# Performance work log

Hardware: AMD Instinct MI355X
Metric: run time of the kernel (lower is better)

Reference implementation:

```python
import jax, jax.numpy as jnp
import numpy as np
import math

N_RAYS = 16384
HIDDEN = 32
Z_BOUNDS = (0.1, 1.0, 10.0)
STEPS_FIRST = (128, 64)
N_IMPORTANCE = 128
ALPHA_IMP = 0.02
INNER, OUTER = 1.0, 2.0


def _uniform_z_log():
    # get_uniform_z_vals: per-segment log10 linspace, endpoint excluded like torch code
    segs = []
    for i in range(len(STEPS_FIRST)):
        lo, hi = math.log10(Z_BOUNDS[i]), math.log10(Z_BOUNDS[i + 1])
        segs.append(np.linspace(lo, hi - (hi - lo) / STEPS_FIRST[i], STEPS_FIRST[i], dtype=np.float32))
    return jnp.asarray(np.concatenate(segs))


def _density(x, Wd1, bd1, Wd2, bd2):
    hfeat = jax.nn.relu(x @ Wd1 + bd1)            # [N,S,HIDDEN]
    sigma = jax.nn.softplus(hfeat @ Wd2 + bd2)[..., 0]  # [N,S]
    return sigma, hfeat


def _mip_scale(x):
    # mipnerf360_scale with translation_center = 0
    dist = jnp.linalg.norm(x, axis=-1, keepdims=True)
    scale = jnp.where(dist > INNER, (OUTER - (OUTER - INNER) / dist) / dist, 1.0)
    return x * scale


def _sample_points(rays_o, rays_d, z_vals):
    pts = rays_o[:, None, :] + rays_d[:, None, :] * z_vals[..., None]  # [N,S,3]
    dirs = rays_d / jnp.linalg.norm(rays_d, axis=-1, keepdims=True)
    return pts, jnp.broadcast_to(dirs[:, None, :], pts.shape)


def _weights_from_sigma(sigmas, z_log):
    # render_rays_log compositing: delta[:, -1] = 0
    delta = jnp.concatenate([z_log[:, 1:] - z_log[:, :-1], jnp.zeros_like(z_log[:, :1])], axis=-1)
    alpha = 1.0 - jnp.exp(-sigmas * delta)
    alpha_shift = jnp.concatenate([jnp.zeros_like(alpha[:, :1]), alpha[:, :-1]], axis=-1)
    weights = alpha * jnp.cumprod(1.0 - alpha_shift, axis=-1)
    return weights


def _reweight(weights):
    z = jnp.zeros_like(weights[:, :1])
    wp = jnp.concatenate([z, weights, z], axis=-1)
    w = 0.5 * (jnp.maximum(wp[:, :-2], wp[:, 1:-1]) + jnp.maximum(wp[:, 1:-1], wp[:, 2:]))
    w = w + ALPHA_IMP / w.shape[-1]
    total = sum(STEPS_FIRST)
    seg_scale = jnp.concatenate([jnp.full((s,), s / total, w.dtype) for s in STEPS_FIRST])
    w = w * seg_scale
    return w / jnp.sum(w, axis=-1, keepdims=True)


def _sample_pdf(z_vals, weights, key):
    n_rays = z_vals.shape[0]
    cdf = jnp.cumsum(weights, axis=-1)
    z_mid = 0.5 * (z_vals[:, :-1] + z_vals[:, 1:])
    u = jnp.linspace(0.0, 1.0 - 1.0 / N_IMPORTANCE, N_IMPORTANCE, dtype=z_vals.dtype)
    u = u[None, :] + jax.random.uniform(key, (n_rays, N_IMPORTANCE), dtype=z_vals.dtype) / N_IMPORTANCE
    u = u * (cdf[:, -2:-1] - cdf[:, 1:2]) + cdf[:, 1:2]
    inds = jax.vmap(lambda c, uu: jnp.searchsorted(c, uu, side='right'))(cdf[:, 1:-2], u) + 1
    g = lambda arr, idx: jnp.take_along_axis(arr, idx, axis=1)
    cdf_b, cdf_a = g(cdf, inds - 1), g(cdf, inds)
    t = (u - cdf_b) / (cdf_a - cdf_b)
    zb, za = g(z_mid, inds - 1), g(z_mid, inds)
    return zb + (za - zb) * t


def _forward(n, h, w, K, E, bg_color, Wd1, bd1, Wd2, bd2, Wc1, bc1, Wc2, bc2):
    # get_rays
    dirs = jnp.stack([w + 0.5, h + 0.5, jnp.ones_like(w)], axis=-1)        # [N,3]
    cam_dirs = dirs @ jnp.linalg.inv(K).T
    rays_d = jnp.einsum('nij,nj->ni', E[:, :3, :3], cam_dirs)
    rays_o = E[:, :3, -1]
    # efficient_sampling (no-grad coarse pass)
    n_rays = rays_o.shape[0]
    z_log_c = jnp.broadcast_to(_uniform_z_log()[None, :], (n_rays, sum(STEPS_FIRST)))
    z_c = jnp.power(10.0, z_log_c)
    xyz_c, _ = _sample_points(rays_o, rays_d, z_c)
    sig_c, _ = _density(_mip_scale(xyz_c), Wd1, bd1, Wd2, bd2)
    w_c = _weights_from_sigma(sig_c, z_log_c)
    w_re = _reweight(w_c)
    z_log_f = jax.lax.stop_gradient(_sample_pdf(z_log_c, w_re, jax.random.key(42)))
    z_f = jnp.power(10.0, z_log_f)
    # fine pass through model
    xyz, dirs_f = _sample_points(rays_o, rays_d, z_f)
    sigma, hfeat = _density(_mip_scale(xyz), Wd1, bd1, Wd2, bd2)
    feat = jnp.concatenate([hfeat, dirs_f], axis=-1)
    rgbs = jax.nn.sigmoid(jax.nn.relu(feat @ Wc1 + bc1) @ Wc2 + bc2)       # [N,S,3]
    weights = _weights_from_sigma(sigma, z_log_f)
    image = jnp.sum(weights[..., None] * rgbs, axis=-2)
    invdepth = jnp.sum(weights / z_f, axis=-1)
    image = image + (1.0 - jnp.sum(weights, axis=-1, keepdims=True)) * bg_color
    lo, hi = math.log10(Z_BOUNDS[0]), math.log10(Z_BOUNDS[-1])
    z_log_s = (z_log_f - lo) / (hi - lo)
    return image, weights, z_log_s, invdepth


def setup_inputs() -> dict:
    key = jax.random.key(0)
    ks = jax.random.split(key, 12)
    N = N_RAYS
    h = jax.random.uniform(ks[0], (N,), dtype=jnp.float32) * 1080.0
    w = jax.random.uniform(ks[1], (N,), dtype=jnp.float32) * 1920.0
    f = 1000.0
    K = jnp.array([[f, 0.0, 960.0], [0.0, f, 540.0], [0.0, 0.0, 1.0]], jnp.float32)
    t = jax.random.normal(ks[2], (N, 3), dtype=jnp.float32) * 0.1
    E = jnp.tile(jnp.eye(4, dtype=jnp.float32)[None], (N, 1, 1)).at[:, :3, 3].set(t)
    n = jax.random.randint(ks[3], (N,), 0, 100)
    bg_color = jax.random.uniform(ks[4], (3,), dtype=jnp.float32)
    Wd1 = jax.random.normal(ks[5], (3, HIDDEN), dtype=jnp.float32) * 0.5
    bd1 = jnp.zeros((HIDDEN,), jnp.float32)
    Wd2 = jax.random.normal(ks[6], (HIDDEN, 1), dtype=jnp.float32) * 0.3
    bd2 = jnp.zeros((1,), jnp.float32)
    Wc1 = jax.random.normal(ks[7], (HIDDEN + 3, HIDDEN), dtype=jnp.float32) * 0.3
    bc1 = jnp.zeros((HIDDEN,), jnp.float32)
    Wc2 = jax.random.normal(ks[8], (HIDDEN, 3), dtype=jnp.float32) * 0.3
    bc2 = jnp.zeros((3,), jnp.float32)
    return {"n": n, "h": h, "w": w, "K": K, "E": E, "bg_color": bg_color,
            "Wd1": Wd1, "bd1": bd1, "Wd2": Wd2, "bd2": bd2,
            "Wc1": Wc1, "bc1": bc1, "Wc2": Wc2, "bc2": bc2}


def reference(n, h, w, K, E, bg_color, Wd1, bd1, Wd2, bd2, Wc1, bc1, Wc2, bc2):
    return _forward(n, h, w, K, E, bg_color, Wd1, bd1, Wd2, bd2, Wc1, bc1, Wc2, bc2)
```

## Files before the change

kernel.cpp:

```cpp
#include <hip/hip_runtime.h>
#include <stdint.h>

#define SC 192
#define SF 128
#define NT 128

#define WD1   0
#define BD1   96
#define WD2   128
#define BD2   160
#define BC2   161
#define NV4   164
#define W24   292
#define SWTOT 420

#define WS_FRAG_OFF 2048
#define WS_NEED     4096

#define RGBS 4

using half8 = __attribute__((ext_vector_type(8))) _Float16;
using f32x4 = __attribute__((ext_vector_type(4))) float;

__device__ __forceinline__ float zlog_c(int t) {
  return (t < 128) ? (-1.0f + (float)t * 0.0078125f)
                   : ((float)(t - 128) * 0.015625f);
}
__device__ __forceinline__ float delta_c(int t) {
  if (t >= SC - 1) return 0.0f;
  return zlog_c(t + 1) - zlog_c(t);
}

__device__ __forceinline__ float fast_rcp(float x) { return __builtin_amdgcn_rcpf(x); }
__device__ __forceinline__ float fast_rsq(float x) { return __builtin_amdgcn_rsqf(x); }
__device__ __forceinline__ float exp10_f(float x) { return __expf(x * 2.30258509299f); }
__device__ __forceinline__ float softplus_f(float x) {
  return fmaxf(x, 0.0f) + __logf(1.0f + __expf(-fabsf(x)));
}

__device__ __forceinline__ uint32_t pk2h(float a, float b) {
  auto p = __builtin_amdgcn_cvt_pkrtz(a, b);
  uint32_t u; __builtin_memcpy(&u, &p, 4); return u;
}
__device__ __forceinline__ unsigned short f2h(float f) {
  _Float16 h = (_Float16)f;
  unsigned short us; __builtin_memcpy(&us, &h, 2); return us;
}

__device__ __forceinline__ float4 ldsf4(const float* p) { return *(const float4*)p; }

__device__ __forceinline__ int hperm(int i, int ntf) {
  return 8 * (i >> 2) + (i & 3) + ntf * 4;
}

__device__ __forceinline__ void threefry2x32_k42(uint32_t& x0, uint32_t& x1) {
  const uint32_t ks0 = 0u, ks1 = 42u;
  const uint32_t ks2 = ks0 ^ ks1 ^ 0x1BD11BDAu;
  const uint32_t ks[3] = {ks0, ks1, ks2};
  const int rot[2][4] = {{13, 15, 26, 6}, {17, 29, 16, 24}};
  x0 += ks[0];
  x1 += ks[1];
#pragma unroll
  for (int i = 0; i < 5; ++i) {
#pragma unroll
    for (int j = 0; j < 4; ++j) {
      x0 += x1;
      const int r = rot[i & 1][j];
      x1 = (x1 << r) | (x1 >> (32 - r));
      x1 ^= x0;
    }
    x0 += ks[(i + 1) % 3];
    x1 += ks[(i + 2) % 3] + (uint32_t)(i + 1);
  }
}

__device__ __forceinline__ float wave_scan_mul(float v, int lane) {
#pragma unroll
  for (int d = 1; d < 64; d <<= 1) {
    float o = __shfl_up(v, d, 64);
    if (lane >= d) v *= o;
  }
  return v;
}
__device__ __forceinline__ float wave_scan_add(float v, int lane) {
#pragma unroll
  for (int d = 1; d < 64; d <<= 1) {
    float o = __shfl_up(v, d, 64);
    if (lane >= d) v += o;
  }
  return v;
}

__global__ __launch_bounds__(NT) void pack_weights(
    const float* __restrict__ Wd1, const float* __restrict__ bd1,
    const float* __restrict__ Wd2, const float* __restrict__ bd2,
    const float* __restrict__ Wc1, const float* __restrict__ bc1,
    const float* __restrict__ Wc2, const float* __restrict__ bc2,
    float* __restrict__ wsf) {
  const int t = threadIdx.x;
  for (int i = t; i < 96; i += NT) wsf[WD1 + i] = Wd1[i];
  for (int i = t; i < 32; i += NT) { wsf[BD1 + i] = bd1[i]; wsf[WD2 + i] = Wd2[i]; }
  if (t == 0) {
    wsf[BD2] = bd2[0];
    wsf[BC2 + 0] = bc2[0]; wsf[BC2 + 1] = bc2[1]; wsf[BC2 + 2] = bc2[2];
  }
  if (t < 32) {
    wsf[NV4 + t * 4 + 0] = bc1[t];
    wsf[NV4 + t * 4 + 1] = Wc1[32 * 32 + t];
    wsf[NV4 + t * 4 + 2] = Wc1[33 * 32 + t];
    wsf[NV4 + t * 4 + 3] = Wc1[34 * 32 + t];
  }
  if (t < 12) {
    const int m = t % 3, q = t / 3;
    uint32_t hw[4];
#pragma unroll
    for (int j2 = 0; j2 < 4; ++j2) {
      const int k0 = q * 8 + j2 * 2;
      hw[j2] = (uint32_t)f2h(Wc2[k0 * 3 + m])
             | ((uint32_t)f2h(Wc2[(k0 + 1) * 3 + m]) << 16);
    }
    ((uint4*)(wsf + W24))[t] = make_uint4(hw[0], hw[1], hw[2], hw[3]);
  }
  if (t < 64) {
    const int q_s = t >> 4;
    const int i = t & 15;
    uint4* frag = (uint4*)((char*)wsf + WS_FRAG_OFF);
#pragma unroll
    for (int nt = 0; nt < 2; ++nt) {
      const int n_s = hperm(i, nt);
      uint32_t hw[4];
#pragma unroll
      for (int j2 = 0; j2 < 4; ++j2) {
        const int k = q_s * 8 + j2 * 2;
        hw[j2] = (uint32_t)f2h(Wc1[k * 32 + n_s])
               | ((uint32_t)f2h(Wc1[(k + 1) * 32 + n_s]) << 16);
      }
      frag[t * 2 + nt] = make_uint4(hw[0], hw[1], hw[2], hw[3]);
    }
  }
}

template <bool USE_WS>
__global__ __launch_bounds__(NT, 8) void nerf_fwd(
    const float* __restrict__ hh, const float* __restrict__ ww,
    const float* __restrict__ K, const float* __restrict__ E,
    const float* __restrict__ bg,
    const float* __restrict__ Wd1, const float* __restrict__ bd1,
    const float* __restrict__ Wd2, const float* __restrict__ bd2,
    const float* __restrict__ Wc1, const float* __restrict__ bc1,
    const float* __restrict__ Wc2, const float* __restrict__ bc2,
    const float* __restrict__ wsf,
    float* __restrict__ out, int n_rays) {
  const int ray = blockIdx.x;
  const int t = threadIdx.x;
  const int lane = t & 63;
  const int wv = t >> 6;
  const int quad = lane >> 4;
  const int m15 = lane & 15;

  __shared__ __align__(16) float sw[SWTOT];
  __shared__ __align__(16) float s_A[32];
  __shared__ __align__(16) float s_B[32];
  __shared__ __align__(16) unsigned char u_buf[3072];
  float*    const s_w   = (float*)u_buf;
  float*    const s_cdf = (float*)(u_buf + 768);
  uint32_t* const s_mm  = (uint32_t*)u_buf;
  float*    const s_sig = (float*)(u_buf + 512);
  float*    const s_rgb = (float*)(u_buf + 1024);
  __shared__ float s_zlf[SF];
  __shared__ float s_tot[8];
  __shared__ float s_red[16];
  float* const s_dv = sw;

  if constexpr (USE_WS) {
    const float4* wsrc = (const float4*)wsf;
    float4* sdst = (float4*)sw;
    for (int i = t; i < SWTOT / 4; i += NT) sdst[i] = wsrc[i];
  } else {
    for (int i = t; i < 96; i += NT) sw[WD1 + i] = Wd1[i];
    for (int i = t; i < 32; i += NT) { sw[BD1 + i] = bd1[i]; sw[WD2 + i] = Wd2[i]; }
    if (t == 0) {
      sw[BD2] = bd2[0];
      sw[BC2 + 0] = bc2[0]; sw[BC2 + 1] = bc2[1]; sw[BC2 + 2] = bc2[2];
    }
    if (t < 32) {
      sw[NV4 + t * 4 + 0] = bc1[t];
      sw[NV4 + t * 4 + 1] = Wc1[32 * 32 + t];
      sw[NV4 + t * 4 + 2] = Wc1[33 * 32 + t];
      sw[NV4 + t * 4 + 3] = Wc1[34 * 32 + t];
    }
    if (t < 12) {
      const int m = t % 3, q = t / 3;
      uint32_t hw[4];
#pragma unroll
      for (int j2 = 0; j2 < 4; ++j2) {
        const int k0 = q * 8 + j2 * 2;
        hw[j2] = (uint32_t)f2h(Wc2[k0 * 3 + m])
               | ((uint32_t)f2h(Wc2[(k0 + 1) * 3 + m]) << 16);
      }
      ((uint4*)(sw + W24))[t] = make_uint4(hw[0], hw[1], hw[2], hw[3]);
    }
  }

  const float k00 = K[0], k01 = K[1], k02 = K[2];
  const float k10 = K[3], k11 = K[4], k12 = K[5];
  const float k20 = K[6], k21 = K[7], k22 = K[8];
  const float det = k00 * (k11 * k22 - k12 * k21)
                  - k01 * (k10 * k22 - k12 * k20)
                  + k02 * (k10 * k21 - k11 * k20);
  const float id = 1.0f / det;
  const float i00 =  (k11 * k22 - k12 * k21) * id;
  const float i01 = -(k01 * k22 - k02 * k21) * id;
  const float i02 =  (k01 * k12 - k02 * k11) * id;
  const float i10 = -(k10 * k22 - k12 * k20) * id;
  const float i11 =  (k00 * k22 - k02 * k20) * id;
  const float i12 = -(k00 * k12 - k02 * k10) * id;
  const float i20 =  (k10 * k21 - k11 * k20) * id;
  const float i21 = -(k00 * k21 - k01 * k20) * id;
  const float i22 =  (k00 * k11 - k01 * k10) * id;

  const float dwx = ww[ray] + 0.5f;
  const float dwy = hh[ray] + 0.5f;
  const float cx = i00 * dwx + i01 * dwy + i02;
  const float cy = i10 * dwx + i11 * dwy + i12;
  const float cz = i20 * dwx + i21 * dwy + i22;
  const float* Er = E + (size_t)ray * 16;
  const float ox = Er[3], oy = Er[7], oz = Er[11];
  const float dx = Er[0] * cx + Er[1] * cy + Er[2] * cz;
  const float dy = Er[4] * cx + Er[5] * cy + Er[6] * cz;
  const float dz = Er[8] * cx + Er[9] * cy + Er[10] * cz;
  const float dd = dx * dx + dy * dy + dz * dz;
  const float inv_nrm = fast_rsq(dd);
  const float ndx = dx * inv_nrm, ndy = dy * inv_nrm, ndz = dz * inv_nrm;
  const float oo  = ox * ox + oy * oy + oz * oz;
  const float od2 = 2.0f * (ox * dx + oy * dy + oz * dz);

  if (t < 32) {
    const float w0 = Wd1[t], w1 = Wd1[32 + t], w2 = Wd1[64 + t];
    s_A[t] = ox * w0 + oy * w1 + oz * w2;
    s_B[t] = dx * w0 + dy * w1 + dz * w2;
  }

  __syncthreads();

  if (t < 32) {
    const float4 nv = ldsf4(sw + NV4 + t * 4);
    s_dv[t] = nv.x + ndx * nv.y + ndy * nv.z + ndz * nv.w;
  }

  const float bd2v = sw[BD2];
  float a0, v0, a1e = 0.0f, v1e = 1.0f;
  {
    float ms0, msz0, ms1 = 0.f, msz1 = 0.f;
    {
      const float z = exp10_f(zlog_c(t));
      const float d2 = fmaf(z, fmaf(z, dd, od2), oo);
      const float r = fast_rsq(fmaxf(d2, 1.0f));
      ms0 = (2.0f - r) * r;
      msz0 = ms0 * z;
    }
    if (wv == 0) {
      const float z = exp10_f((float)t * 0.015625f);
      const float d2 = fmaf(z, fmaf(z, dd, od2), oo);
      const float r = fast_rsq(fmaxf(d2, 1.0f));
      ms1 = (2.0f - r) * r;
      msz1 = ms1 * z;
    }
    float acc0 = bd2v, acc1 = bd2v;
    if (wv == 0) {
#pragma unroll 2
      for (int c = 0; c < 8; ++c) {
        const int k4 = c * 4;
        const float4 A  = ldsf4(s_A + k4);
        const float4 B  = ldsf4(s_B + k4);
        const float4 b  = ldsf4(sw + BD1 + k4);
        const float4 wd = ldsf4(sw + WD2 + k4);
        float v;
        v = fmaf(msz0, B.x, fmaf(ms0, A.x, b.x)); acc0 += fmaxf(v, 0.0f) * wd.x;
        v = fmaf(msz0, B.y, fmaf(ms0, A.y, b.y)); acc0 += fmaxf(v, 0.0f) * wd.y;
        v = fmaf(msz0, B.z, fmaf(ms0, A.z, b.z)); acc0 += fmaxf(v, 0.0f) * wd.z;
        v = fmaf(msz0, B.w, fmaf(ms0, A.w, b.w)); acc0 += fmaxf(v, 0.0f) * wd.w;
        v = fmaf(msz1, B.x, fmaf(ms1, A.x, b.x)); acc1 += fmaxf(v, 0.0f) * wd.x;
        v = fmaf(msz1, B.y, fmaf(ms1, A.y, b.y)); acc1 += fmaxf(v, 0.0f) * wd.y;
        v = fmaf(msz1, B.z, fmaf(ms1, A.z, b.z)); acc1 += fmaxf(v, 0.0f) * wd.z;
        v = fmaf(msz1, B.w, fmaf(ms1, A.w, b.w)); acc1 += fmaxf(v, 0.0f) * wd.w;
      }
    } else {
#pragma unroll 2
      for (int c = 0; c < 8; ++c) {
        const int k4 = c * 4;
        const float4 A  = ldsf4(s_A + k4);
        const float4 B  = ldsf4(s_B + k4);
        const float4 b  = ldsf4(sw + BD1 + k4);
        const float4 wd = ldsf4(sw + WD2 + k4);
        float v;
        v = fmaf(msz0, B.x, fmaf(ms0, A.x, b.x)); acc0 += fmaxf(v, 0.0f) * wd.x;
        v = fmaf(msz0, B.y, fmaf(ms0, A.y, b.y)); acc0 += fmaxf(v, 0.0f) * wd.y;
        v = fmaf(msz0, B.z, fmaf(ms0, A.z, b.z)); acc0 += fmaxf(v, 0.0f) * wd.z;
        v = fmaf(msz0, B.w, fmaf(ms0, A.w, b.w)); acc0 += fmaxf(v, 0.0f) * wd.w;
      }
    }
    v0 = __expf(-softplus_f(acc0) * delta_c(t));
    a0 = 1.0f - v0;
    if (wv == 0) {
      v1e = __expf(-softplus_f(acc1) * delta_c(128 + t));
      a1e = 1.0f - v1e;
    }
  }

  float i0 = wave_scan_mul(v0, lane);
  float i1 = 1.0f;
  if (wv == 0) i1 = wave_scan_mul(v1e, lane);
  if (lane == 63) s_tot[wv] = i0;
  if (wv == 0 && lane == 63) s_tot[2] = i1;
  __syncthreads();
  {
    const float preC1 = s_tot[0];
    const float preC2 = s_tot[0] * s_tot[1];
    float e0x = __shfl_up(i0, 1, 64); if (lane == 0) e0x = 1.0f;
    s_w[t] = a0 * e0x * (wv ? preC1 : 1.0f);
    if (wv == 0) {
      float e1x = __shfl_up(i1, 1, 64); if (lane == 0) e1x = 1.0f;
      s_w[128 + t] = a1e * e1x * preC2;
    }
  }
  __syncthreads();

  float wre0, wre1 = 0.0f;
  {
    const float wm = (t > 0) ? s_w[t - 1] : 0.0f;
    const float w0 = s_w[t];
    const float wp = s_w[t + 1];
    wre0 = 0.5f * (fmaxf(wm, w0) + fmaxf(w0, wp)) + (0.02f / 192.0f);
    wre0 *= (t < 128) ? (128.0f / 192.0f) : (64.0f / 192.0f);
  }
  if (wv == 0) {
    const int e = 128 + t;
    const float wm = s_w[e - 1];
    const float w0 = s_w[e];
    const float wp = (e < SC - 1) ? s_w[e + 1] : 0.0f;
    wre1 = 0.5f * (fmaxf(wm, w0) + fmaxf(w0, wp)) + (0.02f / 192.0f);
    wre1 *= (64.0f / 192.0f);
  }

  float s0 = wave_scan_add(wre0, lane);
  float s1 = 0.0f;
  if (wv == 0) s1 = wave_scan_add(wre1, lane);
  if (lane == 63) s_tot[4 + wv] = s0;
  if (wv == 0 && lane == 63) s_tot[6] = s1;
  __syncthreads();
  {
    const float T0 = s_tot[4], T1 = s_tot[5], T2 = s_tot[6];
    const float inv_total = fast_rcp(T0 + T1 + T2);
    s_cdf[t] = (s0 + (wv ? T0 : 0.0f)) * inv_total;
    if (wv == 0) s_cdf[128 + t] = (s1 + T0 + T1) * inv_total;
  }
  __syncthreads();

  float zlf, zf;
  {
    const uint32_t total = (uint32_t)n_rays * 128u;
    const uint32_t halfc = total >> 1;
    const uint32_t j = (uint32_t)ray * 128u + (uint32_t)t;
    uint32_t x0, x1;
    const bool first = (j < halfc);
    if (first) { x0 = j; x1 = j + halfc; } else { x0 = j - halfc; x1 = j; }
    threefry2x32_k42(x0, x1);
    const uint32_t bits = first ? x0 : x1;
    const float fr = __uint_as_float((bits >> 9) | 0x3f800000u) - 1.0f;

    float u = (float)t * 0.0078125f + fr * 0.0078125f;
    u = u * (s_cdf[190] - s_cdf[1]) + s_cdf[1];

    int lo = 0, hi = 189;
    while (lo < hi) {
      const int mid = (lo + hi) >> 1;
      if (s_cdf[1 + mid] <= u) lo = mid + 1; else hi = mid;
    }
    const int inds = lo + 1;
    const float cb = s_cdf[inds - 1], ca = s_cdf[inds];
    const float tt = (u - cb) * fast_rcp(ca - cb);
    const float zb = 0.5f * (zlog_c(inds - 1) + zlog_c(inds));
    const float za = 0.5f * (zlog_c(inds) + zlog_c(inds + 1));
    zlf = zb + (za - zb) * tt;
    s_zlf[t] = zlf;
    zf = exp10_f(zlf);
  }
  __syncthreads();

  {
    const float d2 = fmaf(zf, fmaf(zf, dd, od2), oo);
    const float r = fast_rsq(fmaxf(d2, 1.0f));
    const float msf = (2.0f - r) * r;
    s_mm[t] = pk2h(msf, msf * zf);
  }

  uint4 BhS0, BhS1, BhS2, BhS3;
  {
    const bool q0 = (quad == 0);
    const int ma = hperm(m15, 0), mb = hperm(m15, 1);
    uint4 fa, fb, fd;
    fa.x = q0 ? pk2h(s_A[ma], s_B[ma]) : 0u;
    fa.y = q0 ? (uint32_t)f2h(sw[BD1 + ma]) : 0u;
    fa.z = 0u; fa.w = 0u;
    fb.x = q0 ? pk2h(s_A[mb], s_B[mb]) : 0u;
    fb.y = q0 ? (uint32_t)f2h(sw[BD1 + mb]) : 0u;
    fb.z = 0u; fb.w = 0u;
    const bool r0 = (m15 == 0);
    fd.x = r0 ? pk2h(sw[WD2 + quad * 8 + 0], sw[WD2 + quad * 8 + 1]) : 0u;
    fd.y = r0 ? pk2h(sw[WD2 + quad * 8 + 2], sw[WD2 + quad * 8 + 3]) : 0u;
    fd.z = r0 ? pk2h(sw[WD2 + quad * 8 + 4], sw[WD2 + quad * 8 + 5]) : 0u;
    fd.w = r0 ? pk2h(sw[WD2 + quad * 8 + 6], sw[WD2 + quad * 8 + 7]) : 0u;
    half8 Waug0, Waug1, WdF;
    __builtin_memcpy(&Waug0, &fa, 16);
    __builtin_memcpy(&Waug1, &fb, 16);
    __builtin_memcpy(&WdF, &fd, 16);

#pragma unroll
    for (int g = 0; g < 4; ++g) {
      const uint32_t mm = s_mm[wv * 64 + g * 16 + m15];
      uint4 bm;
      bm.x = (quad == 0) ? mm : 0u;
      bm.y = (quad == 0) ? 0x00003C00u : 0u;
      bm.z = 0u; bm.w = 0u;
      half8 Bms; __builtin_memcpy(&Bms, &bm, 16);

      f32x4 ad0 = {0.f, 0.f, 0.f, 0.f}, ad1 = {0.f, 0.f, 0.f, 0.f};
      ad0 = __builtin_amdgcn_mfma_f32_16x16x32_f16(Waug0, Bms, ad0, 0, 0, 0);
      ad1 = __builtin_amdgcn_mfma_f32_16x16x32_f16(Waug1, Bms, ad1, 0, 0, 0);

      uint4 bh;
      bh.x = pk2h(fmaxf(ad0[0], 0.0f), fmaxf(ad0[1], 0.0f));
      bh.y = pk2h(fmaxf(ad0[2], 0.0f), fmaxf(ad0[3], 0.0f));
      bh.z = pk2h(fmaxf(ad1[0], 0.0f), fmaxf(ad1[1], 0.0f));
      bh.w = pk2h(fmaxf(ad1[2], 0.0f), fmaxf(ad1[3], 0.0f));
      if (g == 0) BhS0 = bh; else if (g == 1) BhS1 = bh;
      else if (g == 2) BhS2 = bh; else BhS3 = bh;

      half8 Bh; __builtin_memcpy(&Bh, &bh, 16);
      f32x4 as = {0.f, 0.f, 0.f, 0.f};
      as = __builtin_amdgcn_mfma_f32_16x16x32_f16(WdF, Bh, as, 0, 0, 0);
      if (quad == 0) s_sig[wv * 64 + g * 16 + m15] = as[0];
    }
  }
  const float sigf = softplus_f(s_sig[t] + bd2v);

  {
    half8 Whi0, Whi1;
    if constexpr (USE_WS) {
      const uint4* frag = (const uint4*)((const char*)wsf + WS_FRAG_OFF);
      uint4 q0v = frag[lane * 2 + 0];
      uint4 q1v = frag[lane * 2 + 1];
      __builtin_memcpy(&Whi0, &q0v, 16);
      __builtin_memcpy(&Whi1, &q1v, 16);
    } else {
#pragma unroll
      for (int nt = 0; nt < 2; ++nt) {
        const int n_s = hperm(m15, nt);
        uint32_t hw[4];
#pragma unroll
        for (int j2 = 0; j2 < 4; ++j2) {
          const int k = quad * 8 + j2 * 2;
          hw[j2] = (uint32_t)f2h(Wc1[k * 32 + n_s])
                 | ((uint32_t)f2h(Wc1[(k + 1) * 32 + n_s]) << 16);
        }
        uint4 q = make_uint4(hw[0], hw[1], hw[2], hw[3]);
        if (nt == 0) __builtin_memcpy(&Whi0, &q, 16);
        else         __builtin_memcpy(&Whi1, &q, 16);
      }
    }
    const float4 dv0 = ldsf4(s_dv + quad * 8);
    const float4 dv1 = ldsf4(s_dv + quad * 8 + 4);
    uint4 qf = ((const uint4*)(sw + W24))[quad * 3 + (m15 < 3 ? m15 : 0)];
    if (m15 >= 3) qf = make_uint4(0u, 0u, 0u, 0u);
    half8 W2f; __builtin_memcpy(&W2f, &qf, 16);
    const float bc2x = sw[BC2 + 0], bc2y = sw[BC2 + 1], bc2z = sw[BC2 + 2];

#pragma unroll
    for (int g = 0; g < 4; ++g) {
      uint4 bh = (g == 0) ? BhS0 : (g == 1) ? BhS1 : (g == 2) ? BhS2 : BhS3;
      half8 Bh; __builtin_memcpy(&Bh, &bh, 16);

      f32x4 c0 = {0.f, 0.f, 0.f, 0.f}, c1 = {0.f, 0.f, 0.f, 0.f};
      c0 = __builtin_amdgcn_mfma_f32_16x16x32_f16(Whi0, Bh, c0, 0, 0, 0);
      c1 = __builtin_amdgcn_mfma_f32_16x16x32_f16(Whi1, Bh, c1, 0, 0, 0);

      uint4 bw;
      bw.x = pk2h(fmaxf(c0[0] + dv0.x, 0.0f), fmaxf(c0[1] + dv0.y, 0.0f));
      bw.y = pk2h(fmaxf(c0[2] + dv0.z, 0.0f), fmaxf(c0[3] + dv0.w, 0.0f));
      bw.z = pk2h(fmaxf(c1[0] + dv1.x, 0.0f), fmaxf(c1[1] + dv1.y, 0.0f));
      bw.w = pk2h(fmaxf(c1[2] + dv1.z, 0.0f), fmaxf(c1[3] + dv1.w, 0.0f));
      half8 Bav; __builtin_memcpy(&Bav, &bw, 16);

      f32x4 c2 = {0.f, 0.f, 0.f, 0.f};
      c2 = __builtin_amdgcn_mfma_f32_16x16x32_f16(W2f, Bav, c2, 0, 0, 0);
      if (quad == 0) {
        const int scol = wv * 64 + g * 16 + m15;
        float4 px;
        px.x = fast_rcp(1.0f + __expf(-(c2[0] + bc2x)));
        px.y = fast_rcp(1.0f + __expf(-(c2[1] + bc2y)));
        px.z = fast_rcp(1.0f + __expf(-(c2[2] + bc2z)));
        px.w = 0.0f;
        *(float4*)(s_rgb + scol * RGBS) = px;
      }
    }
  }

  const float deltaf = (t < SF - 1) ? (s_zlf[t + 1] - zlf) : 0.0f;
  const float vf = __expf(-sigf * deltaf);
  const float af = 1.0f - vf;
  float fi = wave_scan_mul(vf, lane);
  if (lane == 63) s_tot[wv] = fi;
  __syncthreads();
  float efx = __shfl_up(fi, 1, 64); if (lane == 0) efx = 1.0f;
  const float wf = af * efx * (wv ? s_tot[0] : 1.0f);

  float* o_img = out;
  float* o_w   = out + (size_t)n_rays * 3;
  float* o_z   = out + (size_t)n_rays * (3 + 128);
  float* o_inv = out + (size_t)n_rays * (3 + 256);

  o_w[(size_t)ray * 128 + t] = wf;
  o_z[(size_t)ray * 128 + t] = (zlf + 1.0f) * 0.5f;

  const float4 rgbv = ldsf4(s_rgb + t * RGBS);
  float r0 = wf * rgbv.x;
  float r1 = wf * rgbv.y;
  float r2 = wf * rgbv.z;
  float r3 = wf, r4 = wf * fast_rcp(zf);
#pragma unroll
  for (int d = 32; d > 0; d >>= 1) {
    r0 += __shfl_down(r0, d, 64);
    r1 += __shfl_down(r1, d, 64);
    r2 += __shfl_down(r2, d, 64);
    r3 += __shfl_down(r3, d, 64);
    r4 += __shfl_down(r4, d, 64);
  }
  if (lane == 0) {
    float* p = &s_red[wv * 5];
    p[0] = r0; p[1] = r1; p[2] = r2; p[3] = r3; p[4] = r4;
  }
  __syncthreads();
  if (t == 0) {
    const float accw = s_red[3] + s_red[8];
    const float bgw = 1.0f - accw;
    o_img[(size_t)ray * 3 + 0] = (s_red[0] + s_red[5]) + bgw * bg[0];
    o_img[(size_t)ray * 3 + 1] = (s_red[1] + s_red[6]) + bgw * bg[1];
    o_img[(size_t)ray * 3 + 2] = (s_red[2] + s_red[7]) + bgw * bg[2];
    o_inv[ray] = s_red[4] + s_red[9];
  }
}

extern "C" void kernel_launch(void* const* d_in, const int* in_sizes, int n_in,
                              void* d_out, int out_size, void* d_ws, size_t ws_size,
                              hipStream_t stream) {
  const float* h   = (const float*)d_in[1];
  const float* w   = (const float*)d_in[2];
  const float* K   = (const float*)d_in[3];
  const float* E   = (const float*)d_in[4];
  const float* bg  = (const float*)d_in[5];
  const float* Wd1 = (const float*)d_in[6];
  const float* bd1 = (const float*)d_in[7];
  const float* Wd2 = (const float*)d_in[8];
  const float* bd2 = (const float*)d_in[9];
  const float* Wc1 = (const float*)d_in[10];
  const float* bc1 = (const float*)d_in[11];
  const float* Wc2 = (const float*)d_in[12];
  const float* bc2 = (const float*)d_in[13];
  const int n_rays = in_sizes[1];
  float* wsf = (float*)d_ws;

  if (ws_size >= WS_NEED) {
    pack_weights<<<1, NT, 0, stream>>>(Wd1, bd1, Wd2, bd2, Wc1, bc1, Wc2, bc2, wsf);
    nerf_fwd<true><<<n_rays, NT, 0, stream>>>(h, w, K, E, bg, Wd1, bd1, Wd2, bd2,
                                              Wc1, bc1, Wc2, bc2, wsf,
                                              (float*)d_out, n_rays);
  } else {
    nerf_fwd<false><<<n_rays, NT, 0, stream>>>(h, w, K, E, bg, Wd1, bd1, Wd2, bd2,
                                               Wc1, bc1, Wc2, bc2, nullptr,
                                               (float*)d_out, n_rays);
  }
}
```

Measured before the change: 66.88 us.

## Precompute K inverse, use packed FP32 math, and move RGB sigmoid after compositing

```diff
diff --git a/kernel.cpp b/kernel.cpp
--- a/kernel.cpp
+++ b/kernel.cpp
@@ -12,7 +12,8 @@
 #define BC2   161
 #define NV4   164
 #define W24   292
-#define SWTOT 420
+#define KIV   420
+#define SWTOT 432
 
 #define WS_FRAG_OFF 2048
 #define WS_NEED     4096
@@ -21,6 +22,7 @@
 
 using half8 = __attribute__((ext_vector_type(8))) _Float16;
 using f32x4 = __attribute__((ext_vector_type(4))) float;
+using f32x2 = __attribute__((ext_vector_type(2))) float;
 
 __device__ __forceinline__ float zlog_c(int t) {
   return (t < 128) ? (-1.0f + (float)t * 0.0078125f)
@@ -36,6 +38,17 @@
 __device__ __forceinline__ float exp10_f(float x) { return __expf(x * 2.30258509299f); }
 __device__ __forceinline__ float softplus_f(float x) {
   return fmaxf(x, 0.0f) + __logf(1.0f + __expf(-fabsf(x)));
+}
+
+__device__ __forceinline__ f32x2 pk_fma2(f32x2 a, f32x2 b, f32x2 c) {
+  f32x2 d;
+  asm("v_pk_fma_f32 %0, %1, %2, %3" : "=v"(d) : "v"(a), "v"(b), "v"(c));
+  return d;
+}
+__device__ __forceinline__ f32x2 pk_add2(f32x2 a, f32x2 b) {
+  f32x2 d;
+  asm("v_pk_add_f32 %0, %1, %2" : "=v"(d) : "v"(a), "v"(b));
+  return d;
 }
 
 __device__ __forceinline__ uint32_t pk2h(float a, float b) {
@@ -92,6 +105,7 @@
 }
 
 __global__ __launch_bounds__(NT) void pack_weights(
+    const float* __restrict__ K,
     const float* __restrict__ Wd1, const float* __restrict__ bd1,
     const float* __restrict__ Wd2, const float* __restrict__ bd2,
     const float* __restrict__ Wc1, const float* __restrict__ bc1,
@@ -103,6 +117,22 @@
   if (t == 0) {
     wsf[BD2] = bd2[0];
     wsf[BC2 + 0] = bc2[0]; wsf[BC2 + 1] = bc2[1]; wsf[BC2 + 2] = bc2[2];
+    const float k00 = K[0], k01 = K[1], k02 = K[2];
+    const float k10 = K[3], k11 = K[4], k12 = K[5];
+    const float k20 = K[6], k21 = K[7], k22 = K[8];
+    const float det = k00 * (k11 * k22 - k12 * k21)
+                    - k01 * (k10 * k22 - k12 * k20)
+                    + k02 * (k10 * k21 - k11 * k20);
+    const float id = 1.0f / det;
+    wsf[KIV + 0] =  (k11 * k22 - k12 * k21) * id;
+    wsf[KIV + 1] = -(k01 * k22 - k02 * k21) * id;
+    wsf[KIV + 2] =  (k01 * k12 - k02 * k11) * id;
+    wsf[KIV + 3] = -(k10 * k22 - k12 * k20) * id;
+    wsf[KIV + 4] =  (k00 * k22 - k02 * k20) * id;
+    wsf[KIV + 5] = -(k00 * k12 - k02 * k10) * id;
+    wsf[KIV + 6] =  (k10 * k21 - k11 * k20) * id;
+    wsf[KIV + 7] = -(k00 * k21 - k01 * k20) * id;
+    wsf[KIV + 8] =  (k00 * k11 - k01 * k10) * id;
   }
   if (t < 32) {
     wsf[NV4 + t * 4 + 0] = bc1[t];
@@ -202,22 +232,29 @@
     }
   }
 
-  const float k00 = K[0], k01 = K[1], k02 = K[2];
-  const float k10 = K[3], k11 = K[4], k12 = K[5];
-  const float k20 = K[6], k21 = K[7], k22 = K[8];
-  const float det = k00 * (k11 * k22 - k12 * k21)
-                  - k01 * (k10 * k22 - k12 * k20)
-                  + k02 * (k10 * k21 - k11 * k20);
-  const float id = 1.0f / det;
-  const float i00 =  (k11 * k22 - k12 * k21) * id;
-  const float i01 = -(k01 * k22 - k02 * k21) * id;
-  const float i02 =  (k01 * k12 - k02 * k11) * id;
-  const float i10 = -(k10 * k22 - k12 * k20) * id;
-  const float i11 =  (k00 * k22 - k02 * k20) * id;
-  const float i12 = -(k00 * k12 - k02 * k10) * id;
-  const float i20 =  (k10 * k21 - k11 * k20) * id;
-  const float i21 = -(k00 * k21 - k01 * k20) * id;
-  const float i22 =  (k00 * k11 - k01 * k10) * id;
+  float i00, i01, i02, i10, i11, i12, i20, i21, i22;
+  if constexpr (USE_WS) {
+    i00 = wsf[KIV + 0]; i01 = wsf[KIV + 1]; i02 = wsf[KIV + 2];
+    i10 = wsf[KIV + 3]; i11 = wsf[KIV + 4]; i12 = wsf[KIV + 5];
+    i20 = wsf[KIV + 6]; i21 = wsf[KIV + 7]; i22 = wsf[KIV + 8];
+  } else {
+    const float k00 = K[0], k01 = K[1], k02 = K[2];
+    const float k10 = K[3], k11 = K[4], k12 = K[5];
+    const float k20 = K[6], k21 = K[7], k22 = K[8];
+    const float det = k00 * (k11 * k22 - k12 * k21)
+                    - k01 * (k10 * k22 - k12 * k20)
+                    + k02 * (k10 * k21 - k11 * k20);
+    const float id = 1.0f / det;
+    i00 =  (k11 * k22 - k12 * k21) * id;
+    i01 = -(k01 * k22 - k02 * k21) * id;
+    i02 =  (k01 * k12 - k02 * k11) * id;
+    i10 = -(k10 * k22 - k12 * k20) * id;
+    i11 =  (k00 * k22 - k02 * k20) * id;
+    i12 = -(k00 * k12 - k02 * k10) * id;
+    i20 =  (k10 * k21 - k11 * k20) * id;
+    i21 = -(k00 * k21 - k01 * k20) * id;
+    i22 =  (k00 * k11 - k01 * k10) * id;
+  }
 
   const float dwx = ww[ray] + 0.5f;
   const float dwy = hh[ray] + 0.5f;
@@ -266,7 +303,10 @@
       ms1 = (2.0f - r) * r;
       msz1 = ms1 * z;
     }
-    float acc0 = bd2v, acc1 = bd2v;
+    const f32x2 msp0 = {ms0, ms0}, mszp0 = {msz0, msz0};
+    const f32x2 msp1 = {ms1, ms1}, mszp1 = {msz1, msz1};
+    f32x2 ac0a = {0.f, 0.f}, ac0b = {0.f, 0.f};
+    f32x2 ac1a = {0.f, 0.f}, ac1b = {0.f, 0.f};
     if (wv == 0) {
 #pragma unroll 2
       for (int c = 0; c < 8; ++c) {
@@ -275,15 +315,23 @@
         const float4 B  = ldsf4(s_B + k4);
         const float4 b  = ldsf4(sw + BD1 + k4);
         const float4 wd = ldsf4(sw + WD2 + k4);
-        float v;
-        v = fmaf(msz0, B.x, fmaf(ms0, A.x, b.x)); acc0 += fmaxf(v, 0.0f) * wd.x;
-        v = fmaf(msz0, B.y, fmaf(ms0, A.y, b.y)); acc0 += fmaxf(v, 0.0f) * wd.y;
-        v = fmaf(msz0, B.z, fmaf(ms0, A.z, b.z)); acc0 += fmaxf(v, 0.0f) * wd.z;
-        v = fmaf(msz0, B.w, fmaf(ms0, A.w, b.w)); acc0 += fmaxf(v, 0.0f) * wd.w;
-        v = fmaf(msz1, B.x, fmaf(ms1, A.x, b.x)); acc1 += fmaxf(v, 0.0f) * wd.x;
-        v = fmaf(msz1, B.y, fmaf(ms1, A.y, b.y)); acc1 += fmaxf(v, 0.0f) * wd.y;
-        v = fmaf(msz1, B.z, fmaf(ms1, A.z, b.z)); acc1 += fmaxf(v, 0.0f) * wd.z;
-        v = fmaf(msz1, B.w, fmaf(ms1, A.w, b.w)); acc1 += fmaxf(v, 0.0f) * wd.w;
+        const f32x2 Axy = {A.x, A.y}, Azw = {A.z, A.w};
+        const f32x2 Bxy = {B.x, B.y}, Bzw = {B.z, B.w};
+        const f32x2 bxy = {b.x, b.y}, bzw = {b.z, b.w};
+        const f32x2 wxy = {wd.x, wd.y}, wzw = {wd.z, wd.w};
+        f32x2 p;
+        p = pk_fma2(mszp0, Bxy, pk_fma2(msp0, Axy, bxy));
+        p.x = fmaxf(p.x, 0.f); p.y = fmaxf(p.y, 0.f);
+        ac0a = pk_fma2(p, wxy, ac0a);
+        p = pk_fma2(mszp0, Bzw, pk_fma2(msp0, Azw, bzw));
+        p.x = fmaxf(p.x, 0.f); p.y = fmaxf(p.y, 0.f);
+        ac0b = pk_fma2(p, wzw, ac0b);
+        p = pk_fma2(mszp1, Bxy, pk_fma2(msp1, Axy, bxy));
+        p.x = fmaxf(p.x, 0.f); p.y = fmaxf(p.y, 0.f);
+        ac1a = pk_fma2(p, wxy, ac1a);
+        p = pk_fma2(mszp1, Bzw, pk_fma2(msp1, Azw, bzw));
+        p.x = fmaxf(p.x, 0.f); p.y = fmaxf(p.y, 0.f);
+        ac1b = pk_fma2(p, wzw, ac1b);
       }
     } else {
 #pragma unroll 2
@@ -293,16 +341,24 @@
         const float4 B  = ldsf4(s_B + k4);
         const float4 b  = ldsf4(sw + BD1 + k4);
         const float4 wd = ldsf4(sw + WD2 + k4);
-        float v;
-        v = fmaf(msz0, B.x, fmaf(ms0, A.x, b.x)); acc0 += fmaxf(v, 0.0f) * wd.x;
-        v = fmaf(msz0, B.y, fmaf(ms0, A.y, b.y)); acc0 += fmaxf(v, 0.0f) * wd.y;
-        v = fmaf(msz0, B.z, fmaf(ms0, A.z, b.z)); acc0 += fmaxf(v, 0.0f) * wd.z;
-        v = fmaf(msz0, B.w, fmaf(ms0, A.w, b.w)); acc0 += fmaxf(v, 0.0f) * wd.w;
+        const f32x2 Axy = {A.x, A.y}, Azw = {A.z, A.w};
+        const f32x2 Bxy = {B.x, B.y}, Bzw = {B.z, B.w};
+        const f32x2 bxy = {b.x, b.y}, bzw = {b.z, b.w};
+        const f32x2 wxy = {wd.x, wd.y}, wzw = {wd.z, wd.w};
+        f32x2 p;
+        p = pk_fma2(mszp0, Bxy, pk_fma2(msp0, Axy, bxy));
+        p.x = fmaxf(p.x, 0.f); p.y = fmaxf(p.y, 0.f);
+        ac0a = pk_fma2(p, wxy, ac0a);
+        p = pk_fma2(mszp0, Bzw, pk_fma2(msp0, Azw, bzw));
+        p.x = fmaxf(p.x, 0.f); p.y = fmaxf(p.y, 0.f);
+        ac0b = pk_fma2(p, wzw, ac0b);
       }
     }
+    const float acc0 = bd2v + ((ac0a.x + ac0a.y) + (ac0b.x + ac0b.y));
     v0 = __expf(-softplus_f(acc0) * delta_c(t));
     a0 = 1.0f - v0;
     if (wv == 0) {
+      const float acc1 = bd2v + ((ac1a.x + ac1a.y) + (ac1b.x + ac1b.y));
       v1e = __expf(-softplus_f(acc1) * delta_c(128 + t));
       a1e = 1.0f - v1e;
     }
@@ -474,7 +530,6 @@
     uint4 qf = ((const uint4*)(sw + W24))[quad * 3 + (m15 < 3 ? m15 : 0)];
     if (m15 >= 3) qf = make_uint4(0u, 0u, 0u, 0u);
     half8 W2f; __builtin_memcpy(&W2f, &qf, 16);
-    const float bc2x = sw[BC2 + 0], bc2y = sw[BC2 + 1], bc2z = sw[BC2 + 2];
 
 #pragma unroll
     for (int g = 0; g < 4; ++g) {
@@ -496,12 +551,7 @@
       c2 = __builtin_amdgcn_mfma_f32_16x16x32_f16(W2f, Bav, c2, 0, 0, 0);
       if (quad == 0) {
         const int scol = wv * 64 + g * 16 + m15;
-        float4 px;
-        px.x = fast_rcp(1.0f + __expf(-(c2[0] + bc2x)));
-        px.y = fast_rcp(1.0f + __expf(-(c2[1] + bc2y)));
-        px.z = fast_rcp(1.0f + __expf(-(c2[2] + bc2z)));
-        px.w = 0.0f;
-        *(float4*)(s_rgb + scol * RGBS) = px;
+        *(f32x4*)(s_rgb + scol * RGBS) = c2;
       }
     }
   }
@@ -523,22 +573,29 @@
   o_w[(size_t)ray * 128 + t] = wf;
   o_z[(size_t)ray * 128 + t] = (zlf + 1.0f) * 0.5f;
 
+  const float bc2x = sw[BC2 + 0], bc2y = sw[BC2 + 1], bc2z = sw[BC2 + 2];
   const float4 rgbv = ldsf4(s_rgb + t * RGBS);
-  float r0 = wf * rgbv.x;
-  float r1 = wf * rgbv.y;
-  float r2 = wf * rgbv.z;
-  float r3 = wf, r4 = wf * fast_rcp(zf);
+  const float sr = fast_rcp(1.0f + __expf(-(rgbv.x + bc2x)));
+  const float sg = fast_rcp(1.0f + __expf(-(rgbv.y + bc2y)));
+  const float sb = fast_rcp(1.0f + __expf(-(rgbv.z + bc2z)));
+
+  f32x2 p01 = {wf * sr, wf * sg};
+  f32x2 p23 = {wf * sb, wf};
+  float r4 = wf * fast_rcp(zf);
 #pragma unroll
   for (int d = 32; d > 0; d >>= 1) {
-    r0 += __shfl_down(r0, d, 64);
-    r1 += __shfl_down(r1, d, 64);
-    r2 += __shfl_down(r2, d, 64);
-    r3 += __shfl_down(r3, d, 64);
+    f32x2 o01, o23;
+    o01.x = __shfl_down(p01.x, d, 64);
+    o01.y = __shfl_down(p01.y, d, 64);
+    o23.x = __shfl_down(p23.x, d, 64);
+    o23.y = __shfl_down(p23.y, d, 64);
+    p01 = pk_add2(p01, o01);
+    p23 = pk_add2(p23, o23);
     r4 += __shfl_down(r4, d, 64);
   }
   if (lane == 0) {
     float* p = &s_red[wv * 5];
-    p[0] = r0; p[1] = r1; p[2] = r2; p[3] = r3; p[4] = r4;
+    p[0] = p01.x; p[1] = p01.y; p[2] = p23.x; p[3] = p23.y; p[4] = r4;
   }
   __syncthreads();
   if (t == 0) {
@@ -571,7 +628,7 @@
   float* wsf = (float*)d_ws;
 
   if (ws_size >= WS_NEED) {
-    pack_weights<<<1, NT, 0, stream>>>(Wd1, bd1, Wd2, bd2, Wc1, bc1, Wc2, bc2, wsf);
+    pack_weights<<<1, NT, 0, stream>>>(K, Wd1, bd1, Wd2, bd2, Wc1, bc1, Wc2, bc2, wsf);
     nerf_fwd<true><<<n_rays, NT, 0, stream>>>(h, w, K, E, bg, Wd1, bd1, Wd2, bd2,
                                               Wc1, bc1, Wc2, bc2, wsf,
                                               (float*)d_out, n_rays);
```

New measurement: 65.15 us. 1.03x faster.
